# Performance work log

Hardware: AMD Instinct MI355X
Metric: run time of the kernel (lower is better)

The kernel has to match this reference:

```python
import jax, jax.numpy as jnp
import numpy as np

N = 100000   # number of octree nodes at this depth
K = 27       # kernel_size '333' -> 3*3*3 neighbors
C = 128      # feature channels


def setup_inputs() -> dict:
    key = jax.random.key(0)
    k1, k2 = jax.random.split(key)
    data = jax.random.normal(k1, (N, C), dtype=jnp.float32)
    # neighbor indices in [-1, N); -1 marks invalid (empty/boundary) neighbors
    neigh = jax.random.randint(k2, (N, K), -1, N, dtype=jnp.int64)
    return {"data": data, "neigh": neigh}


def reference(data, neigh):
    # Fused masked gather: treat neigh == -1 as zero-fill.
    # Equivalent to: out = zeros([N,K,C]); out[valid] = data[neigh[valid]]
    valid = neigh >= 0                      # [N, K]
    idx = jnp.where(valid, neigh, 0)        # safe indices
    gathered = data[idx]                    # [N, K, C]
    return jnp.where(valid[..., None], gathered, jnp.zeros((), dtype=data.dtype))
```

## Files before the change

kernel.cpp:

```cpp
#include <hip/hip_runtime.h>
#include <climits>


typedef float floatx4 __attribute__((ext_vector_type(4)));

constexpr int ROWS_PER_CHUNK = 8192;
constexpr int THREADS = 256;
constexpr int BLOCKS  = 2048;
constexpr int WAVES   = BLOCKS * THREADS / 64;
constexpr int GPW     = 6;

__global__ __launch_bounds__(THREADS) void octree2col_chunked(
    const floatx4* __restrict__ data,
    const int*     __restrict__ neigh,
    floatx4*       __restrict__ out,
    int rows_total,
    int n_data_rows)
{
    const int wave = (blockIdx.x * THREADS + threadIdx.x) >> 6;
    const int lane = threadIdx.x & 63;
    const int half = lane >> 5;
    const int c4   = lane & 31;

    const int ngroups = (rows_total + 63) >> 6;
    const int nchunks = (n_data_rows + ROWS_PER_CHUNK - 1) / ROWS_PER_CHUNK;

    int nv[GPW];
    int gbase[GPW];
#pragma unroll
    for (int i = 0; i < GPW; ++i) {
        const int g = wave + i * WAVES;
        gbase[i] = g << 6;
        const int row = gbase[i] + lane;
        nv[i] = (g < ngroups && row < rows_total) ? neigh[row] : INT_MIN;
    }

#pragma unroll
    for (int i = 0; i < GPW; ++i) {
        unsigned long long zm = __ballot(nv[i] == -1);
        while (zm) {
            int r1 = __builtin_ctzll(zm); zm &= zm - 1;
            int r2 = -1;
            if (zm) { r2 = __builtin_ctzll(zm); zm &= zm - 1; }
            const int r = half ? r2 : r1;
            if (r >= 0) {
                const long long row = gbase[i] + r;
                floatx4 z = {0.f, 0.f, 0.f, 0.f};
                __builtin_nontemporal_store(z, &out[row * 32 + c4]);
            }
        }
    }

    for (int p = 0; p < nchunks; ++p) {
        const int lo = p * ROWS_PER_CHUNK;
#pragma unroll
        for (int i = 0; i < GPW; ++i) {
            unsigned long long m =
                __ballot((unsigned)(nv[i] - lo) < (unsigned)ROWS_PER_CHUNK);
            while (m) {
                int r1 = __builtin_ctzll(m); m &= m - 1;
                int r2 = -1;
                if (m) { r2 = __builtin_ctzll(m); m &= m - 1; }
                const int r  = half ? r2 : r1;
                const int rs = r < 0 ? 0 : r;
                const int idx = __shfl(nv[i], rs);
                if (r >= 0) {
                    const long long row = gbase[i] + r;
                    floatx4 v = data[(long long)idx * 32 + c4];
                    __builtin_nontemporal_store(v, &out[row * 32 + c4]);
                }
            }
        }
        __syncthreads();
    }
}

extern "C" void kernel_launch(void* const* d_in, const int* in_sizes, int n_in,
                              void* d_out, int out_size, void* d_ws, size_t ws_size,
                              hipStream_t stream) {
    const floatx4* data  = (const floatx4*)d_in[0];
    const int*     neigh = (const int*)d_in[1];
    floatx4*       out   = (floatx4*)d_out;

    const int rows_total  = in_sizes[1];
    const int n_data_rows = in_sizes[0] / 128;

    octree2col_chunked<<<BLOCKS, THREADS, 0, stream>>>(
        data, neigh, out, rows_total, n_data_rows);
}
```

Before: 330.5 us.

## Bin neighbor pairs by source chunk, then copy per-XCD bins

Replaces the repeated chunk-scan kernel with a two-phase scheme. First a binning kernel counting-sorts (row, index) pairs into fixed-capacity buckets of 2048 source rows and writes zero rows directly. Then a copy kernel maps bins to XCDs by block index, so each XCD's L2 holds a small working set of source rows. This removes the per-chunk rescans and the block-wide barriers. In exchange it adds an extra workspace pass plus two extra launches, needs a large workspace, and uses a slow per-thread overflow path when a bucket fills.

```diff
diff --git a/kernel.cpp b/kernel.cpp
--- a/kernel.cpp
+++ b/kernel.cpp
@@ -4,37 +4,122 @@
 
 typedef float floatx4 __attribute__((ext_vector_type(4)));
 
+constexpr int CH_LOG     = 11;
+constexpr int K1_THREADS = 1024;
+constexpr int K2_BLOCKS  = 2048;
+constexpr int K2_THREADS = 256;
+
+__global__ void k_zero(int* __restrict__ cursor, int NB) {
+    if ((int)threadIdx.x < NB) cursor[threadIdx.x] = 0;
+}
+
+__global__ __launch_bounds__(K1_THREADS) void k_bin(
+    const int* __restrict__ neigh,
+    const floatx4* __restrict__ data,
+    floatx4*   __restrict__ out,
+    int2*      __restrict__ pairs,
+    int*       __restrict__ cursor,
+    int R, int NB, int cap)
+{
+    extern __shared__ int lds[];
+    int* l_cnt  = lds;
+    int* l_base = lds + NB;
+    for (int i = threadIdx.x; i < NB; i += K1_THREADS) l_cnt[i] = 0;
+    __syncthreads();
+
+    const int r = blockIdx.x * K1_THREADS + threadIdx.x;
+    int idx = INT_MIN, b = 0, rank = 0;
+    if (r < R) {
+        idx = neigh[r];
+        if (idx >= 0) {
+            b = idx >> CH_LOG;
+            rank = atomicAdd(&l_cnt[b], 1);
+        }
+    }
+    __syncthreads();
+    for (int i = threadIdx.x; i < NB; i += K1_THREADS)
+        l_base[i] = atomicAdd(&cursor[i], l_cnt[i]);
+    __syncthreads();
+
+    if (idx >= 0) {
+        const int slot = l_base[b] + rank;
+        if (slot < cap) {
+            pairs[(size_t)b * cap + slot] = make_int2(r, idx);
+        } else {
+            const floatx4* s = data + (size_t)idx * 32;
+            floatx4*       d = out  + (size_t)r   * 32;
+            for (int c = 0; c < 32; ++c) __builtin_nontemporal_store(s[c], &d[c]);
+        }
+    } else if (idx == -1) {
+        const floatx4 z = {0.f, 0.f, 0.f, 0.f};
+        floatx4* d = out + (size_t)r * 32;
+        for (int c = 0; c < 32; ++c) __builtin_nontemporal_store(z, &d[c]);
+    }
+}
+
+__global__ __launch_bounds__(K2_THREADS) void k_copy(
+    const floatx4* __restrict__ data,
+    floatx4*       __restrict__ out,
+    const int2*    __restrict__ pairs,
+    const int*     __restrict__ cursor,
+    int NB, int cap)
+{
+    const int hw   = threadIdx.x >> 5;
+    const int c4   = threadIdx.x & 31;
+    const int xcd  = blockIdx.x & 7;
+    const int lblk = blockIdx.x >> 3;
+
+    const int NB_full = NB & ~7;
+
+    for (int b = xcd; b < NB_full; b += 8) {
+        int cnt = cursor[b]; if (cnt > cap) cnt = cap;
+        const int lo = (int)(((long long)cnt * lblk)       >> 8);
+        const int hi = (int)(((long long)cnt * (lblk + 1)) >> 8);
+        const int2* pb = pairs + (size_t)b * cap;
+        for (int e = lo + hw; e < hi; e += 8) {
+            const int2 pr = pb[e];
+            const floatx4 v = data[(size_t)pr.y * 32 + c4];
+            __builtin_nontemporal_store(v, &out[(size_t)pr.x * 32 + c4]);
+        }
+    }
+    for (int b = NB_full; b < NB; ++b) {
+        int cnt = cursor[b]; if (cnt > cap) cnt = cap;
+        const int lo = (int)((long long)cnt * blockIdx.x       / K2_BLOCKS);
+        const int hi = (int)((long long)cnt * (blockIdx.x + 1) / K2_BLOCKS);
+        const int2* pb = pairs + (size_t)b * cap;
+        for (int e = lo + hw; e < hi; e += 8) {
+            const int2 pr = pb[e];
+            const floatx4 v = data[(size_t)pr.y * 32 + c4];
+            __builtin_nontemporal_store(v, &out[(size_t)pr.x * 32 + c4]);
+        }
+    }
+}
+
 constexpr int ROWS_PER_CHUNK = 8192;
-constexpr int THREADS = 256;
-constexpr int BLOCKS  = 2048;
-constexpr int WAVES   = BLOCKS * THREADS / 64;
-constexpr int GPW     = 6;
+constexpr int FB_THREADS = 256;
+constexpr int FB_BLOCKS  = 2048;
+constexpr int FB_WAVES   = FB_BLOCKS * FB_THREADS / 64;
+constexpr int GPW        = 6;
 
-__global__ __launch_bounds__(THREADS) void octree2col_chunked(
-    const floatx4* __restrict__ data,
-    const int*     __restrict__ neigh,
-    floatx4*       __restrict__ out,
-    int rows_total,
-    int n_data_rows)
+__global__ __launch_bounds__(FB_THREADS) void octree2col_chunked(
+    const floatx4* __restrict__ data, const int* __restrict__ neigh,
+    floatx4* __restrict__ out, int rows_total, int n_data_rows)
 {
-    const int wave = (blockIdx.x * THREADS + threadIdx.x) >> 6;
+    const int wave = (blockIdx.x * FB_THREADS + threadIdx.x) >> 6;
     const int lane = threadIdx.x & 63;
     const int half = lane >> 5;
     const int c4   = lane & 31;
-
     const int ngroups = (rows_total + 63) >> 6;
     const int nchunks = (n_data_rows + ROWS_PER_CHUNK - 1) / ROWS_PER_CHUNK;
 
-    int nv[GPW];
-    int gbase[GPW];
+    int nv[GPW]; int gbase[GPW];
 #pragma unroll
     for (int i = 0; i < GPW; ++i) {
-        const int g = wave + i * WAVES;
+        const int g = wave + i * FB_WAVES;
         gbase[i] = g << 6;
         const int row = gbase[i] + lane;
         nv[i] = (g < ngroups && row < rows_total) ? neigh[row] : INT_MIN;
     }
-
 #pragma unroll
     for (int i = 0; i < GPW; ++i) {
         unsigned long long zm = __ballot(nv[i] == -1);
@@ -50,7 +135,6 @@
             }
         }
     }
-
     for (int p = 0; p < nchunks; ++p) {
         const int lo = p * ROWS_PER_CHUNK;
 #pragma unroll
@@ -82,9 +166,30 @@
     const int*     neigh = (const int*)d_in[1];
     floatx4*       out   = (floatx4*)d_out;
 
-    const int rows_total  = in_sizes[1];
-    const int n_data_rows = in_sizes[0] / 128;
+    const int R = in_sizes[1];
+    const int N = in_sizes[0] / 128;
+    const int NB = (N + (1 << CH_LOG) - 1) >> CH_LOG;
 
-    octree2col_chunked<<<BLOCKS, THREADS, 0, stream>>>(
-        data, neigh, out, rows_total, n_data_rows);
+    long long mean = (((long long)R << CH_LOG) + N - 1) / N;
+    int cap = (int)((mean * 5 + 3) / 4);
+    cap = (cap + 63) & ~63;
+    const size_t need = 1024 + (size_t)NB * (size_t)cap * sizeof(int2);
+
+    if (ws_size >= need && NB <= 1024) {
+        int*  cursor = (int*)d_ws;
+        int2* pairs  = (int2*)((char*)d_ws + 1024);
+
+        k_zero<<<1, 1024, 0, stream>>>(cursor, NB);
+
+        const int k1_blocks = (R + K1_THREADS - 1) / K1_THREADS;
+        const size_t lds = 2 * (size_t)NB * sizeof(int);
+        k_bin<<<k1_blocks, K1_THREADS, lds, stream>>>(
+            neigh, data, out, pairs, cursor, R, NB, cap);
+
+        k_copy<<<K2_BLOCKS, K2_THREADS, 0, stream>>>(
+            data, out, pairs, cursor, NB, cap);
+    } else {
+        octree2col_chunked<<<FB_BLOCKS, FB_THREADS, 0, stream>>>(
+            data, neigh, out, R, N);
+    }
 }
```

Result: no change. 328.4 us, median of 2 (-0.6%).
